# Kernel optimization log

Measured on AMD Instinct MI355X. Metric: run time of the kernel, lower is better.

## Reference

```python
import jax, jax.numpy as jnp
import numpy as np

B, S, IN, H, OUT = 64, 512, 1024, 512, 512
EPS = 1e-5
ADAPTIVE_RATE = 0.01


def setup_inputs() -> dict:
    key = jax.random.key(0)
    ks = iter(jax.random.split(key, 64))

    def rn(shape, scale):
        return (jax.random.normal(next(ks), shape, jnp.float32) * scale)

    d = {}
    d["x"] = jax.random.normal(next(ks), (B, S, IN), jnp.float32)
    d["context"] = jax.random.normal(next(ks), (B, H), jnp.float32)
    d["state_importance"] = jnp.ones((1, H), jnp.float32)
    # embedding
    d["W_emb"], d["b_emb"] = rn((H, IN), 0.02), rn((H,), 0.01)
    # core layers: Linear + BatchNorm1d (gamma=1, beta=0 torch init)
    d["W0"], d["b0"] = rn((H, H), 0.03), rn((H,), 0.01)
    d["g0"], d["bt0"] = jnp.ones((H,), jnp.float32), jnp.zeros((H,), jnp.float32)
    d["W1"], d["b1"] = rn((H, H), 0.03), rn((H,), 0.01)
    d["g1"], d["bt1"] = jnp.ones((H,), jnp.float32), jnp.zeros((H,), jnp.float32)
    # two LSTMCells (hidden -> hidden), torch gate order i,f,g,o
    lstm_scale = 1.0 / np.sqrt(H)
    for l in range(2):
        d[f"Wih{l}"] = rn((4 * H, H), lstm_scale)
        d[f"Whh{l}"] = rn((4 * H, H), lstm_scale)
        d[f"bih{l}"] = rn((4 * H,), lstm_scale)
        d[f"bhh{l}"] = rn((4 * H,), lstm_scale)
    # compression gate: Linear(2H, H) + LayerNorm + Sigmoid
    d["Wc"], d["bc"] = rn((H, 2 * H), 0.02), rn((H,), 0.01)
    d["lnc_g"], d["lnc_b"] = jnp.ones((H,), jnp.float32), jnp.zeros((H,), jnp.float32)
    # importance generator: Linear, ReLU, Linear, LayerNorm, Sigmoid
    d["Wi1"], d["bi1"] = rn((H, H), 0.03), rn((H,), 0.01)
    d["Wi2"], d["bi2"] = rn((H, H), 0.03), rn((H,), 0.01)
    d["lni_g"], d["lni_b"] = jnp.ones((H,), jnp.float32), jnp.zeros((H,), jnp.float32)
    # final layer
    d["Wf"], d["bf"] = rn((OUT, H), 0.03), rn((OUT,), 0.01)
    return d


def _bn_channel_dim1(h, gamma, beta):
    # BatchNorm1d (training mode) on (B, S, H) with channel dim = dim 1 (S == num_features)
    m = h.mean(axis=(0, 2), keepdims=True)
    v = h.var(axis=(0, 2), keepdims=True)  # biased, like torch normalization
    return gamma[None, :, None] * (h - m) / jnp.sqrt(v + EPS) + beta[None, :, None]


def _ln(h, g, b):
    m = h.mean(-1, keepdims=True)
    v = h.var(-1, keepdims=True)
    return g * (h - m) / jnp.sqrt(v + EPS) + b


def _lstm_cell(xt, h, c, Wih, Whh, bih, bhh):
    z = xt @ Wih.T + bih + h @ Whh.T + bhh  # (B, 4H)
    i, f, g, o = jnp.split(z, 4, axis=-1)
    c = jax.nn.sigmoid(f) * c + jax.nn.sigmoid(i) * jnp.tanh(g)
    h = jax.nn.sigmoid(o) * jnp.tanh(c)
    return h, c


def reference(x, context, state_importance, W_emb, b_emb,
              W0, b0, g0, bt0, W1, b1, g1, bt1,
              Wih0, Whh0, bih0, bhh0, Wih1, Whh1, bih1, bhh1,
              Wc, bc, lnc_g, lnc_b, Wi1, bi1, Wi2, bi2, lni_g, lni_b,
              Wf, bf):
    h = x @ W_emb.T + b_emb  # (B, S, H)
    h = jax.nn.relu(_bn_channel_dim1(h @ W0.T + b0, g0, bt0))
    h = jax.nn.relu(_bn_channel_dim1(h @ W1.T + b1, g1, bt1))

    # stacked 2-layer LSTMCell over the sequence, keep only the final hidden
    zeros = jnp.zeros((B, H), h.dtype)

    def step(carry, xt):
        h0, c0, h1, c1 = carry
        h0, c0 = _lstm_cell(xt, h0, c0, Wih0, Whh0, bih0, bhh0)
        h1, c1 = _lstm_cell(h0, h1, c1, Wih1, Whh1, bih1, bhh1)
        return (h0, c0, h1, c1), None

    (h0, c0, h1, c1), _ = jax.lax.scan(step, (zeros, zeros, zeros, zeros),
                                       jnp.swapaxes(h, 0, 1))
    processed = h1  # (B, H)

    comp = jax.nn.sigmoid(_ln(jnp.concatenate([processed, context], axis=-1) @ Wc.T + bc,
                              lnc_g, lnc_b))
    compressed = processed * comp

    imp = jax.nn.sigmoid(_ln(jax.nn.relu(compressed @ Wi1.T + bi1) @ Wi2.T + bi2,
                             lni_g, lni_b))
    si_new = state_importance + ADAPTIVE_RATE * (
        jnp.abs(imp).mean(axis=0, keepdims=True) - state_importance)

    out = compressed @ Wf.T + bf
    return out, si_new
```

## Files before the change

### kernel.cpp

```cpp
#include <hip/hip_runtime.h>
#include <hip/hip_bf16.h>
#include <stdint.h>


typedef __attribute__((ext_vector_type(8))) short short8;
typedef __attribute__((ext_vector_type(4))) float floatx4;
typedef __attribute__((ext_vector_type(2))) unsigned uintx2;

__device__ inline float b2f(short u){
  union { float f; uint32_t i; } x; x.i = ((uint32_t)(uint16_t)u) << 16; return x.f;
}
__device__ inline short f2b(float f){
  union { float f; uint32_t i; } x; x.f = f;
  uint32_t r = (x.i + 0x7FFFu + ((x.i >> 16) & 1u)) >> 16;
  return (short)(uint16_t)r;
}
__device__ inline float sigm(float x){ return 1.0f / (1.0f + __expf(-x)); }

__device__ inline float blk_sum(float v, float* red){
  #pragma unroll
  for (int o = 32; o > 0; o >>= 1) v += __shfl_down(v, o, 64);
  int wv = threadIdx.x >> 6;
  __syncthreads();
  if ((threadIdx.x & 63) == 0) red[wv] = v;
  __syncthreads();
  return red[0] + red[1] + red[2] + red[3];
}

__device__ inline void stage16(const short* g, short* l){
  __builtin_amdgcn_global_load_lds(
      (const __attribute__((address_space(1))) void*)(uintptr_t)g,
      (__attribute__((address_space(3))) void*)(uintptr_t)l,
      16, 0, 0);
}

__device__ inline int ldsLoadAcq(int* p){
  return __hip_atomic_load(p, __ATOMIC_ACQUIRE, __HIP_MEMORY_SCOPE_WORKGROUP);
}
__device__ inline void ldsStoreRel(int* p, int v){
  __hip_atomic_store(p, v, __ATOMIC_RELEASE, __HIP_MEMORY_SCOPE_WORKGROUP);
}
__device__ inline int ldsAddRel(int* p){
  return __hip_atomic_fetch_add(p, 1, __ATOMIC_RELEASE, __HIP_MEMORY_SCOPE_WORKGROUP);
}


__global__ void set_flag(const unsigned* __restrict__ si_bits, unsigned* __restrict__ flag){
  if (threadIdx.x == 0 && blockIdx.x == 0)
    *flag = (si_bits[0] == 0x3F800000u) ? 1u : 0u;
}


__global__ __launch_bounds__(256) void convq(
    const unsigned* __restrict__ flag, int mode,
    const void* s0, long e0, short* d0, int n0,
    const void* s1, long e1, short* d1, int n1,
    const void* s2, long e2, short* d2, int n2,
    const void* s3, long e3, short* d3, int n3)
{
  const bool isf32 = (*flag != 0u);
  const int gid = blockIdx.x*256 + threadIdx.x;
  const int stride = gridDim.x*256;
  const void* ss[4] = {s0,s1,s2,s3};
  long ee[4]  = {e0,e1,e2,e3};
  short* dd[4] = {d0,d1,d2,d3};
  int nn[4]   = {n0,n1,n2,n3};
  for (int s = 0; s < 4; s++){
    if (!dd[s]) continue;
    if (mode == 1) {
      if (!isf32) continue;
      for (int i = gid; i < nn[s]; i += stride)
        dd[s][i] = ((const short*)ss[s])[ee[s] + i];
    } else if (isf32) {
      for (int i = gid; i < nn[s]; i += stride)
        dd[s][i] = f2b(((const float*)ss[s])[ee[s] + i]);
    } else {
      for (int i = gid; i < nn[s]; i += stride)
        dd[s][i] = ((const short*)ss[s])[ee[s] + i];
    }
  }
}


__global__ __launch_bounds__(256) void gemm_bt(
    const short* __restrict__ A, const short* __restrict__ A2, int splitRow,
    int lda, const short* __restrict__ W, const short* __restrict__ bias,
    short* __restrict__ C, int ldc, int row0, int K)
{
  __shared__ alignas(16) short As[128*32];
  __shared__ alignas(16) short Bs[128*32];
  const int tid  = threadIdx.x;
  const int lane = tid & 63;
  const int wave = tid >> 6;
  const int wm = wave >> 1, wn = wave & 1;
  const int bm = blockIdx.x, bn = blockIdx.y;
  const int R0 = row0 + bm*128;
  const short* Ab = (R0 < splitRow) ? A2 : A;

  floatx4 acc[4][4];
  #pragma unroll
  for (int i = 0; i < 4; i++)
    #pragma unroll
    for (int j = 0; j < 4; j++){ floatx4 z = {0.f,0.f,0.f,0.f}; acc[i][j] = z; }

  const short* Ag = Ab + (size_t)(R0 + (tid >> 2))*lda + (tid & 3)*8;
  const short* Wg = W  + (size_t)(bn*128 + (tid >> 2))*K + (tid & 3)*8;

  const int kk  = (lane >> 4) * 8;
  const int rA  = wm*64 + (lane & 15);
  const int rB  = wn*64 + (lane & 15);

  for (int k0 = 0; k0 < K; k0 += 32) {
    __syncthreads();
    stage16(Ag + k0,                  As + tid*8);
    stage16(Ag + k0 + (size_t)64*lda, As + 2048 + tid*8);
    stage16(Wg + k0,                  Bs + tid*8);
    stage16(Wg + k0 + (size_t)64*K,   Bs + 2048 + tid*8);
    __syncthreads();

    short8 af[4], bf[4];
    #pragma unroll
    for (int i = 0; i < 4; i++){
      af[i] = *(const short8*)&As[(rA + i*16)*32 + kk];
      bf[i] = *(const short8*)&Bs[(rB + i*16)*32 + kk];
    }
    #pragma unroll
    for (int i = 0; i < 4; i++)
      #pragma unroll
      for (int j = 0; j < 4; j++)
        acc[i][j] = __builtin_amdgcn_mfma_f32_16x16x32_bf16(af[i], bf[j], acc[i][j], 0, 0, 0);
  }

  const int crow0 = R0 + wm*64 + (lane >> 4)*4;
  const int ccol0 = bn*128 + wn*64;
  #pragma unroll
  for (int i = 0; i < 4; i++){
    #pragma unroll
    for (int j = 0; j < 4; j++){
      int col = ccol0 + j*16 + (lane & 15);
      float bv = b2f(bias[col]);
      #pragma unroll
      for (int r = 0; r < 4; r++){
        int row = crow0 + i*16 + r;
        C[(size_t)row*ldc + col] = f2b(acc[i][j][r] + bv);
      }
    }
  }
}


__global__ __launch_bounds__(256) void bn_relu(
    const short* __restrict__ X, const short* __restrict__ gamma,
    const short* __restrict__ beta, short* __restrict__ Y)
{
  const int s = blockIdx.x, tid = threadIdx.x;
  __shared__ float red[4];
  float s1 = 0.f, s2 = 0.f;
  for (int i = tid; i < 4096; i += 256){
    int b = i >> 6, c = i & 63;
    short8 v = *(const short8*)(X + ((size_t)(b*512 + s))*512 + c*8);
    #pragma unroll
    for (int u = 0; u < 8; u++){ float f = b2f(v[u]); s1 += f; s2 += f*f; }
  }
  s1 = blk_sum(s1, red);
  s2 = blk_sum(s2, red);
  float mean = s1 * (1.f/32768.f);
  float var  = fmaxf(s2 * (1.f/32768.f) - mean*mean, 0.f);
  float sc = b2f(gamma[s]) * rsqrtf(var + 1e-5f);
  float sh = b2f(beta[s]) - mean * sc;
  for (int i = tid; i < 4096; i += 256){
    int b = i >> 6, c = i & 63;
    size_t base = ((size_t)(b*512 + s))*512 + c*8;
    short8 v = *(const short8*)(X + base);
    short8 o;
    #pragma unroll
    for (int u = 0; u < 8; u++){
      float f = b2f(v[u]) * sc + sh;
      o[u] = f2b(fmaxf(f, 0.f));
    }
    *(short8*)(Y + base) = o;
  }
}


__global__ __launch_bounds__(256, 1) void lstm_persist(
    const short* __restrict__ Xseq,
    const short* __restrict__ Wih0, const short* __restrict__ Whh0,
    const short* __restrict__ bih0, const short* __restrict__ bhh0,
    const short* __restrict__ Wih1, const short* __restrict__ Whh1,
    const short* __restrict__ bih1, const short* __restrict__ bhh1,
    short* __restrict__ h0r,
    short* __restrict__ h1r,
    unsigned* __restrict__ f0,
    unsigned* __restrict__ f1,
    unsigned* __restrict__ ep0,
    unsigned* __restrict__ ep1)
{
  const int wg   = blockIdx.x;
  const int tid  = threadIdx.x;
  const int lane = tid & 63;
  const int wave = tid >> 6;

  if (wg == 64){
    if (wave >= 2) return;
    const unsigned* sp = (wave == 0 ? f0 : f1) + lane*16;
    unsigned* dp = (wave == 0 ? ep0 : ep1) + lane*16;
    for (unsigned itv = 1; itv <= 512; ++itv){
      for (;;){
        unsigned v;
        asm volatile("global_load_dword %0, %1, off sc1\n\t"
                     "s_waitcnt vmcnt(0)"
                     : "=v"(v) : "v"(sp) : "memory");
        if (__all((int)(v >= itv))) break;
      }
      asm volatile("global_store_dword %0, %1, off sc0 sc1"
                   :: "v"(dp), "v"(itv) : "memory");
    }
    return;
  }

  const int l15  = lane & 15;
  const int quad = lane >> 4;
  const int kq   = quad * 8;

  __shared__ float zp0[2*2*64*33];
  __shared__ float zp1[2*2*64*33];
  __shared__ alignas(16) short xpf[512];
  __shared__ int go0, go1, zc0, zc1, gc0, gc1;
  #define ZPL0(p,t,r,c) zp0[((((p)*2+(t))*64) + (r))*33 + (c)]
  #define ZPL1(p,t,r,c) zp1[((((p)*2+(t))*64) + (r))*33 + (c)]

  if (tid == 0){ go0 = -1; go1 = -1; zc0 = 0; zc1 = 0; gc0 = 0; gc1 = 0; }
  __syncthreads();

  const short* Wt = (wave==0) ? Wih0 : (wave==1) ? Whh0 : (wave==2) ? Wih1 : Whh1;
  short8 wreg[2][16];
  #pragma unroll
  for (int nt = 0; nt < 2; nt++){
    int g2 = nt*2 + (l15 >> 3);
    int ml = l15 & 7;
    const short* wrow = Wt + (size_t)(g2*512 + wg*8 + ml)*512 + kq;
    #pragma unroll
    for (int kk = 0; kk < 16; kk++)
      wreg[nt][kk] = *(const short8*)(wrow + kk*32);
  }

  const int lp  = wave >> 1;
  const int t2  = tid & 127;
  const int bbg = t2 >> 1;
  const int m4  = (t2 & 1) * 4;
  const short* biA = lp ? bih1 : bih0;
  const short* bhA = lp ? bhh1 : bhh0;
  float bsL[4][4];
  #pragma unroll
  for (int g = 0; g < 4; g++)
    #pragma unroll
    for (int j = 0; j < 4; j++){
      int m = wg*8 + m4 + j;
      bsL[g][j] = b2f(biA[g*512+m]) + b2f(bhA[g*512+m]);
    }
  float cst[4] = {0.f, 0.f, 0.f, 0.f};

  for (int it = 0; it <= 512; ++it){
    const bool act = (wave==0) ? (it < 512)
                   : (wave==1) ? (it >= 1 && it < 512)
                   : (wave==2) ? (it >= 1)
                   :             (it >= 2);

    if (wave == 1 && it >= 1){
      const unsigned want = (unsigned)it;
      const unsigned* p = ep0 + wg*16;
      for (;;){
        unsigned v;
        asm volatile("global_load_dword %0, %1, off sc1\n\t"
                     "s_waitcnt vmcnt(0)"
                     : "=v"(v) : "v"(p) : "memory");
        if (v >= want) break;
      }
      __builtin_amdgcn_sched_barrier(0);
      if (lane == 0) ldsStoreRel(&go0, it);
    }
    if (wave == 3){
      if (it >= 2){
        const unsigned want = (unsigned)it;
        const unsigned* p = ep1 + wg*16;
        for (;;){
          unsigned v;
          asm volatile("global_load_dword %0, %1, off sc1\n\t"
                       "s_waitcnt vmcnt(0)"
                       : "=v"(v) : "v"(p) : "memory");
          if (v >= want) break;
        }
        __builtin_amdgcn_sched_barrier(0);
      }
      if (lane == 0) ldsStoreRel(&go1, it);
    }
    if (wave == 2 && it >= 1){
      while (ldsLoadAcq(&go0) < it) { }
      __builtin_amdgcn_sched_barrier(0);
    }

    floatx4 acc[4][2];
    #pragma unroll
    for (int mt = 0; mt < 4; mt++)
      #pragma unroll
      for (int nt = 0; nt < 2; nt++){ floatx4 z = {0.f,0.f,0.f,0.f}; acc[mt][nt] = z; }

    if (act){
      const short* Ab;
      size_t rstride;
      if (wave == 0)      { Ab = Xseq + (size_t)it*512;               rstride = 262144; }
      else if (wave <= 2) { Ab = h0r + (size_t)((it-1)&1)*32768;      rstride = 512; }
      else                { Ab = h1r + (size_t)(it&1)*32768;          rstride = 512; }
      const short* ap[4];
      #pragma unroll
      for (int mt = 0; mt < 4; mt++)
        ap[mt] = Ab + (size_t)(mt*16 + l15)*rstride + kq;

      if (wave == 0){
        #pragma unroll
        for (int kk = 0; kk < 16; kk++){
          short8 af[4];
          #pragma unroll
          for (int mt = 0; mt < 4; mt++) af[mt] = *(const short8*)(ap[mt] + kk*32);
          #pragma unroll
          for (int mt = 0; mt < 4; mt++){
            acc[mt][0] = __builtin_amdgcn_mfma_f32_16x16x32_bf16(af[mt], wreg[0][kk], acc[mt][0], 0, 0, 0);
            acc[mt][1] = __builtin_amdgcn_mfma_f32_16x16x32_bf16(af[mt], wreg[1][kk], acc[mt][1], 0, 0, 0);
          }
        }
      } else {
        short8 hb[2][4][4];
        #pragma unroll
        for (int pb = 0; pb < 2; pb++)
          #pragma unroll
          for (int kk = 0; kk < 4; kk++)
            #pragma unroll
            for (int mt = 0; mt < 4; mt++)
              asm volatile("global_load_dwordx4 %0, %1, off sc1"
                           : "=v"(hb[pb][kk][mt])
                           : "v"(ap[mt] + (pb*4 + kk)*32));
        #pragma unroll
        for (int kb = 0; kb < 4; kb++){
          const int cur = kb & 1;
          if (kb < 3) asm volatile("s_waitcnt vmcnt(16)" ::: "memory");
          else        asm volatile("s_waitcnt vmcnt(0)"  ::: "memory");
          __builtin_amdgcn_sched_barrier(0);
          #pragma unroll
          for (int kk = 0; kk < 4; kk++)
            #pragma unroll
            for (int mt = 0; mt < 4; mt++){
              acc[mt][0] = __builtin_amdgcn_mfma_f32_16x16x32_bf16(hb[cur][kk][mt], wreg[0][kb*4+kk], acc[mt][0], 0, 0, 0);
              acc[mt][1] = __builtin_amdgcn_mfma_f32_16x16x32_bf16(hb[cur][kk][mt], wreg[1][kb*4+kk], acc[mt][1], 0, 0, 0);
            }
          if (kb < 2){
            #pragma unroll
            for (int kk = 0; kk < 4; kk++)
              #pragma unroll
              for (int mt = 0; mt < 4; mt++)
                asm volatile("global_load_dwordx4 %0, %1, off sc1"
                             : "=v"(hb[cur][kk][mt])
                             : "v"(ap[mt] + ((kb+2)*4 + kk)*32));
          }
        }
      }
    }

    const int par = it & 1;
    if (wave < 2){
      if (it < 512){
        if (it >= 2) while (ldsLoadAcq(&gc0) < 2*(it-1)) { }
        #pragma unroll
        for (int mt = 0; mt < 4; mt++)
          #pragma unroll
          for (int nt = 0; nt < 2; nt++)
            #pragma unroll
            for (int r = 0; r < 4; r++)
              ZPL0(par, wave, mt*16 + quad*4 + r, nt*16 + l15) = acc[mt][nt][r];
        if (lane == 0) ldsAddRel(&zc0);
      }
    } else {
      if (it >= 1){
        if (it >= 3) while (ldsLoadAcq(&gc1) < 2*(it-2)) { }
        #pragma unroll
        for (int mt = 0; mt < 4; mt++)
          #pragma unroll
          for (int nt = 0; nt < 2; nt++)
            #pragma unroll
            for (int r = 0; r < 4; r++)
              ZPL1(par, wave-2, mt*16 + quad*4 + r, nt*16 + l15) = acc[mt][nt][r];
        if (lane == 0) ldsAddRel(&zc1);
      }
    }

    if (wave < 2){
      if (it < 512){
        while (ldsLoadAcq(&zc0) < 2*(it+1)) { }
        if (it >= 2) while (ldsLoadAcq(&go1) < it) { }
        float hv[4];
        #pragma unroll
        for (int j = 0; j < 4; j++){
          int ml = m4 + j;
          float zi = ZPL0(par,0,bbg,      ml) + ZPL0(par,1,bbg,      ml) + bsL[0][j];
          float zf = ZPL0(par,0,bbg,  8 + ml) + ZPL0(par,1,bbg,  8 + ml) + bsL[1][j];
          float zg = ZPL0(par,0,bbg, 16 + ml) + ZPL0(par,1,bbg, 16 + ml) + bsL[2][j];
          float zo = ZPL0(par,0,bbg, 24 + ml) + ZPL0(par,1,bbg, 24 + ml) + bsL[3][j];
          cst[j] = sigm(zf)*cst[j] + sigm(zi)*tanhf(zg);
          hv[j] = sigm(zo)*tanhf(cst[j]);
        }
        uintx2 d;
        d.x = (unsigned)(uint16_t)f2b(hv[0]) | ((unsigned)(uint16_t)f2b(hv[1]) << 16);
        d.y = (unsigned)(uint16_t)f2b(hv[2]) | ((unsigned)(uint16_t)f2b(hv[3]) << 16);
        short* dst = h0r + (size_t)par*32768 + bbg*512 + wg*8 + m4;
        asm volatile("global_store_dwordx2 %0, %1, off sc0 sc1" :: "v"(dst), "v"(d) : "memory");
        asm volatile("s_waitcnt vmcnt(0)" ::: "memory");
        __builtin_amdgcn_sched_barrier(0);
        if (lane == 0){
          int old = ldsAddRel(&gc0);
          if (old == 2*it + 1){
            unsigned nv = (unsigned)(it + 1);
            asm volatile("global_store_dword %0, %1, off sc0 sc1"
                         :: "v"(f0 + wg*16), "v"(nv) : "memory");
          }
        }
      }
      if (wave == 0 && it + 2 < 512){
        const short* nx = Xseq + (size_t)(it + 2)*512 + lane*8;
        #pragma unroll 8
        for (int r = 0; r < 64; ++r)
          stage16(nx + (size_t)r*262144, xpf);
      }
    } else {
      if (it >= 1){
        while (ldsLoadAcq(&zc1) < 2*it) { }
        float hv[4];
        #pragma unroll
        for (int j = 0; j < 4; j++){
          int ml = m4 + j;
          float zi = ZPL1(par,0,bbg,      ml) + ZPL1(par,1,bbg,      ml) + bsL[0][j];
          float zf = ZPL1(par,0,bbg,  8 + ml) + ZPL1(par,1,bbg,  8 + ml) + bsL[1][j];
          float zg = ZPL1(par,0,bbg, 16 + ml) + ZPL1(par,1,bbg, 16 + ml) + bsL[2][j];
          float zo = ZPL1(par,0,bbg, 24 + ml) + ZPL1(par,1,bbg, 24 + ml) + bsL[3][j];
          cst[j] = sigm(zf)*cst[j] + sigm(zi)*tanhf(zg);
          hv[j] = sigm(zo)*tanhf(cst[j]);
        }
        uintx2 d;
        d.x = (unsigned)(uint16_t)f2b(hv[0]) | ((unsigned)(uint16_t)f2b(hv[1]) << 16);
        d.y = (unsigned)(uint16_t)f2b(hv[2]) | ((unsigned)(uint16_t)f2b(hv[3]) << 16);
        short* dst = h1r + (size_t)((it-1)&1)*32768 + bbg*512 + wg*8 + m4;
        asm volatile("global_store_dwordx2 %0, %1, off sc0 sc1" :: "v"(dst), "v"(d) : "memory");
        asm volatile("s_waitcnt vmcnt(0)" ::: "memory");
        __builtin_amdgcn_sched_barrier(0);
        if (lane == 0){
          int old = ldsAddRel(&gc1);
          if (old == 2*it - 1){
            unsigned nv = (unsigned)(it + 1);
            asm volatile("global_store_dword %0, %1, off sc0 sc1"
                         :: "v"(f1 + wg*16), "v"(nv) : "memory");
          }
        }
      }
    }
  }
  #undef ZPL0
  #undef ZPL1
}


__global__ __launch_bounds__(256) void head_gate_out(
    const short* __restrict__ h1, const short* __restrict__ ctx,
    const short* __restrict__ Wc, const short* __restrict__ bc,
    const short* __restrict__ lng, const short* __restrict__ lnb,
    const short* __restrict__ Wf, const short* __restrict__ bfb,
    short* __restrict__ compressed, void* __restrict__ outp,
    const unsigned* __restrict__ flag)
{
  const int b = blockIdx.x, tid = threadIdx.x;
  const bool isf32 = (*flag != 0u);
  __shared__ float xc[1024];
  __shared__ float cv[512];
  __shared__ float red[4];
  for (int i = tid; i < 512; i += 256) xc[i]       = b2f(h1 [b*512 + i]);
  for (int i = tid; i < 512; i += 256) xc[512 + i] = b2f(ctx[b*512 + i]);
  __syncthreads();
  float y[2];
  #pragma unroll
  for (int jj = 0; jj < 2; jj++){
    int j = tid + jj*256;
    const short* wr = Wc + (size_t)j*1024;
    float a = 0.f;
    for (int k = 0; k < 1024; k += 8){
      short8 wv = *(const short8*)(wr + k);
      #pragma unroll
      for (int u = 0; u < 8; u++) a += b2f(wv[u]) * xc[k + u];
    }
    y[jj] = a + b2f(bc[j]);
  }
  float s = blk_sum(y[0] + y[1], red);
  float mean = s * (1.f/512.f);
  float q = (y[0]-mean)*(y[0]-mean) + (y[1]-mean)*(y[1]-mean);
  q = blk_sum(q, red);
  float inv = rsqrtf(q * (1.f/512.f) + 1e-5f);
  #pragma unroll
  for (int jj = 0; jj < 2; jj++){
    int j = tid + jj*256;
    float v = (y[jj]-mean)*inv*b2f(lng[j]) + b2f(lnb[j]);
    float cm = xc[j] * sigm(v);
    cv[j] = cm;
    compressed[(size_t)b*512 + j] = f2b(cm);
  }
  __syncthreads();
  #pragma unroll
  for (int jj = 0; jj < 2; jj++){
    int j = tid + jj*256;
    const short* wr = Wf + (size_t)j*512;
    float a = 0.f;
    for (int k = 0; k < 512; k += 8){
      short8 wv = *(const short8*)(wr + k);
      #pragma unroll
      for (int u = 0; u < 8; u++) a += b2f(wv[u]) * cv[k + u];
    }
    float o = a + b2f(bfb[j]);
    if (isf32) ((float*)outp)[(size_t)b*512 + j] = o;
    else       ((short*)outp)[(size_t)b*512 + j] = f2b(o);
  }
}


__global__ __launch_bounds__(256) void head_imp(
    const short* __restrict__ compressed,
    const short* __restrict__ Wi1, const short* __restrict__ bi1,
    const short* __restrict__ Wi2, const short* __restrict__ bi2,
    const short* __restrict__ lng, const short* __restrict__ lnb,
    float* __restrict__ imp)
{
  const int b = blockIdx.x, tid = threadIdx.x;
  __shared__ float xr[512];
  __shared__ float t1[512];
  __shared__ float red[4];
  for (int i = tid; i < 512; i += 256) xr[i] = b2f(compressed[b*512 + i]);
  __syncthreads();
  #pragma unroll
  for (int jj = 0; jj < 2; jj++){
    int j = tid + jj*256;
    const short* wr = Wi1 + (size_t)j*512;
    float a = 0.f;
    for (int k = 0; k < 512; k += 8){
      short8 wv = *(const short8*)(wr + k);
      #pragma unroll
      for (int u = 0; u < 8; u++) a += b2f(wv[u]) * xr[k + u];
    }
    t1[j] = fmaxf(a + b2f(bi1[j]), 0.f);
  }
  __syncthreads();
  float y[2];
  #pragma unroll
  for (int jj = 0; jj < 2; jj++){
    int j = tid + jj*256;
    const short* wr = Wi2 + (size_t)j*512;
    float a = 0.f;
    for (int k = 0; k < 512; k += 8){
      short8 wv = *(const short8*)(wr + k);
      #pragma unroll
      for (int u = 0; u < 8; u++) a += b2f(wv[u]) * t1[k + u];
    }
    y[jj] = a + b2f(bi2[j]);
  }
  float s = blk_sum(y[0] + y[1], red);
  float mean = s * (1.f/512.f);
  float q = (y[0]-mean)*(y[0]-mean) + (y[1]-mean)*(y[1]-mean);
  q = blk_sum(q, red);
  float inv = rsqrtf(q * (1.f/512.f) + 1e-5f);
  #pragma unroll
  for (int jj = 0; jj < 2; jj++){
    int j = tid + jj*256;
    imp[(size_t)b*512 + j] = sigm((y[jj]-mean)*inv*b2f(lng[j]) + b2f(lnb[j]));
  }
}


__global__ __launch_bounds__(256) void head_si(
    const float* __restrict__ imp, const short* __restrict__ si,
    void* __restrict__ outp, const unsigned* __restrict__ flag)
{
  int tid = threadIdx.x;
  const bool isf32 = (*flag != 0u);
  #pragma unroll
  for (int mm = 0; mm < 2; mm++){
    int m = tid + mm*256;
    float s = 0.f;
    for (int b = 0; b < 64; b++) s += fabsf(imp[(size_t)b*512 + m]);
    float mean = s * (1.f/64.f);
    float sv = b2f(si[m]);
    float o = sv + 0.01f*(mean - sv);
    if (isf32) ((float*)outp)[32768 + m] = o;
    else       ((short*)outp)[32768 + m] = f2b(o);
  }
}


extern "C" void kernel_launch(void* const* d_in, const int* in_sizes, int n_in,
                              void* d_out, int out_size, void* d_ws, size_t ws_size,
                              hipStream_t stream)
{
  (void)in_sizes; (void)n_in; (void)out_size; (void)ws_size;
  char* ws = (char*)d_ws;
  unsigned* f0b    = (unsigned*)(ws);
  unsigned* f1b    = (unsigned*)(ws + 4096);
  unsigned* ep0b   = (unsigned*)(ws + 8192);
  unsigned* ep1b   = (unsigned*)(ws + 12288);
  unsigned* flag   = (unsigned*)(ws + 16384);
  short*    xStage = (short*)(ws + 20480);
  short*    ring   = (short*)(ws + 282624);
  short*    comp   = (short*)(ws + 806912);
  float*    impb   = (float*)(ws + 872448);
  short*    SA     = (short*)(ws + 1003520);

  short* h0r = ring;
  short* h1r = ring + 65536;

  short* aWemb = SA + 0;
  short* aW0   = SA + 524288;
  short* aW1   = SA + 786432;
  short* aWih0 = SA + 1048576;
  short* aWhh0 = SA + 2097152;
  short* aWih1 = SA + 3145728;
  short* aWhh1 = SA + 4194304;
  short* aWc   = SA + 5242880;
  short* aWi1  = SA + 5767168;
  short* aWi2  = SA + 6029312;
  short* aWf   = SA + 6291456;
  short* V     = SA + 6553600;
  short* abemb = V + 0;     short* ab0  = V + 512;   short* ag0  = V + 1024;
  short* abt0  = V + 1536;  short* ab1  = V + 2048;  short* ag1  = V + 2560;
  short* abt1  = V + 3072;  short* abih0= V + 3584;  short* abhh0= V + 5632;
  short* abih1 = V + 7680;  short* abhh1= V + 9728;  short* abc  = V + 11776;
  short* alncg = V + 12288; short* alncb= V + 12800; short* abi1 = V + 13312;
  short* abi2  = V + 13824; short* alnig= V + 14336; short* alnib= V + 14848;
  short* abfb  = V + 15360; short* actx = V + 15872; short* asi  = V + 48640;

  short* xb  = (short*)d_in[0];
  short* hL0 = xb + 16777216;

  hipMemsetAsync(ws, 0, 16384, stream);
  set_flag<<<1, 64, 0, stream>>>((const unsigned*)d_in[2], flag);

  dim3 blk(256);
  convq<<<256, blk, 0, stream>>>(flag, 0,
      d_in[0], 0, xStage, 65536, nullptr,0,nullptr,0, nullptr,0,nullptr,0, nullptr,0,nullptr,0);
  for (long n0 = 65536; n0 < 33554432; n0 <<= 1) {
    int blocks = (int)((n0 + 1023) / 1024); if (blocks > 4096) blocks = 4096;
    convq<<<blocks, blk, 0, stream>>>(flag, 0,
        d_in[0], n0, xb + n0, (int)n0, nullptr,0,nullptr,0, nullptr,0,nullptr,0, nullptr,0,nullptr,0);
  }
  convq<<<64, blk, 0, stream>>>(flag, 1,
      xStage, 0, xb, 65536, nullptr,0,nullptr,0, nullptr,0,nullptr,0, nullptr,0,nullptr,0);

  convq<<<1024, blk, 0, stream>>>(flag, 0,
      d_in[3], 0, aWemb, 524288,  d_in[5], 0, aW0, 262144,
      d_in[9], 0, aW1,   262144,  d_in[21],0, aWc, 524288);
  convq<<<2048, blk, 0, stream>>>(flag, 0,
      d_in[13],0, aWih0, 1048576, d_in[14],0, aWhh0, 1048576,
      d_in[17],0, aWih1, 1048576, d_in[18],0, aWhh1, 1048576);
  convq<<<1024, blk, 0, stream>>>(flag, 0,
      d_in[25],0, aWi1, 262144,   d_in[27],0, aWi2, 262144,
      d_in[31],0, aWf,  262144,   d_in[1], 0, actx, 32768);
  convq<<<8, blk, 0, stream>>>(flag, 0,
      d_in[4], 0, abemb, 512,  d_in[6], 0, ab0, 512,
      d_in[7], 0, ag0,   512,  d_in[8], 0, abt0, 512);
  convq<<<8, blk, 0, stream>>>(flag, 0,
      d_in[10],0, ab1, 512,  d_in[11],0, ag1, 512,
      d_in[12],0, abt1,512,  d_in[22],0, abc, 512);
  convq<<<8, blk, 0, stream>>>(flag, 0,
      d_in[15],0, abih0, 2048,  d_in[16],0, abhh0, 2048,
      d_in[19],0, abih1, 2048,  d_in[20],0, abhh1, 2048);
  convq<<<8, blk, 0, stream>>>(flag, 0,
      d_in[23],0, alncg, 512,  d_in[24],0, alncb, 512,
      d_in[26],0, abi1,  512,  d_in[28],0, abi2,  512);
  convq<<<8, blk, 0, stream>>>(flag, 0,
      d_in[29],0, alnig, 512,  d_in[30],0, alnib, 512,
      d_in[32],0, abfb,  512,  d_in[2], 0, asi,   512);

  gemm_bt<<<dim3(1, 4), blk, 0, stream>>>(xb, xb, 0, 1024, aWemb, abemb,
                                          xStage, 512, 0, 1024);
  for (int r0 = 128; r0 < 32768; r0 <<= 1) {
    gemm_bt<<<dim3(r0/128, 4), blk, 0, stream>>>(xb, xb, 0, 1024, aWemb, abemb,
                                                 xb, 512, r0, 1024);
  }
  gemm_bt<<<dim3(256, 4), blk, 0, stream>>>(xb, xStage, 128, 512, aW0, ab0,
                                            hL0, 512, 0, 512);
  bn_relu<<<512, blk, 0, stream>>>(hL0, ag0, abt0, hL0);
  gemm_bt<<<dim3(256, 4), blk, 0, stream>>>(hL0, hL0, 0, 512, aW1, ab1,
                                            xb, 512, 0, 512);
  bn_relu<<<512, blk, 0, stream>>>(xb, ag1, abt1, xb);

  lstm_persist<<<65, blk, 0, stream>>>(xb, aWih0, aWhh0, abih0, abhh0,
                                       aWih1, aWhh1, abih1, abhh1,
                                       h0r, h1r, f0b, f1b, ep0b, ep1b);

  head_gate_out<<<64, blk, 0, stream>>>(h1r + 32768, actx, aWc, abc, alncg, alncb,
                                        aWf, abfb, comp, d_out, flag);
  head_imp<<<64, blk, 0, stream>>>(comp, aWi1, abi1, aWi2, abi2, alnig, alnib, impb);
  head_si<<<1, blk, 0, stream>>>(impb, asi, d_out, flag);
}
```

Before: 6.796 ms.

## Replace aggregator-block barrier with direct per-wave flag polling in LSTM

Removes the extra relay workgroup that gathered per-block completion flags and rebroadcast epoch counters. Each producing wave now writes its own flag into a transposed flag matrix, and consumer waves poll all 64 blocks' flags directly with vector loads and a wave-wide all-reduce. The h0 ring grows from 2 to 4 slots so the layer-0 writer can run further ahead of the layer-1 reader, which relaxes the h1go wait. This takes one hop off the global barrier latency per step. In exchange, every consumer wave issues more polling traffic and the ring needs more memory.

After: 7.991 ms. +17.6%, slower.

```diff
diff --git a/kernel.cpp b/kernel.cpp
--- a/kernel.cpp
+++ b/kernel.cpp
@@ -191,34 +191,13 @@
     const short* __restrict__ bih1, const short* __restrict__ bhh1,
     short* __restrict__ h0r,
     short* __restrict__ h1r,
-    unsigned* __restrict__ f0,
-    unsigned* __restrict__ f1,
-    unsigned* __restrict__ ep0,
-    unsigned* __restrict__ ep1)
+    unsigned* __restrict__ fblk0,
+    unsigned* __restrict__ fblk1)
 {
   const int wg   = blockIdx.x;
   const int tid  = threadIdx.x;
   const int lane = tid & 63;
   const int wave = tid >> 6;
-
-  if (wg == 64){
-    if (wave >= 2) return;
-    const unsigned* sp = (wave == 0 ? f0 : f1) + lane*16;
-    unsigned* dp = (wave == 0 ? ep0 : ep1) + lane*16;
-    for (unsigned itv = 1; itv <= 512; ++itv){
-      for (;;){
-        unsigned v;
-        asm volatile("global_load_dword %0, %1, off sc1\n\t"
-                     "s_waitcnt vmcnt(0)"
-                     : "=v"(v) : "v"(sp) : "memory");
-        if (__all((int)(v >= itv))) break;
-      }
-      asm volatile("global_store_dword %0, %1, off sc0 sc1"
-                   :: "v"(dp), "v"(itv) : "memory");
-    }
-    return;
-  }
-
   const int l15  = lane & 15;
   const int quad = lane >> 4;
   const int kq   = quad * 8;
@@ -226,11 +205,11 @@
   __shared__ float zp0[2*2*64*33];
   __shared__ float zp1[2*2*64*33];
   __shared__ alignas(16) short xpf[512];
-  __shared__ int go0, go1, zc0, zc1, gc0, gc1;
+  __shared__ int h1go, zc0, zc1, gd0, gd1;
   #define ZPL0(p,t,r,c) zp0[((((p)*2+(t))*64) + (r))*33 + (c)]
   #define ZPL1(p,t,r,c) zp1[((((p)*2+(t))*64) + (r))*33 + (c)]
 
-  if (tid == 0){ go0 = -1; go1 = -1; zc0 = 0; zc1 = 0; gc0 = 0; gc1 = 0; }
+  if (tid == 0){ h1go = -1; zc0 = 0; zc1 = 0; gd0 = 0; gd1 = 0; }
   __syncthreads();
 
   const short* Wt = (wave==0) ? Wih0 : (wave==1) ? Whh0 : (wave==2) ? Wih1 : Whh1;
@@ -261,43 +240,39 @@
     }
   float cst[4] = {0.f, 0.f, 0.f, 0.f};
 
+  const unsigned* poll0 = fblk0 + wg*128 + lane*2;
+  const unsigned* poll1 = fblk1 + wg*128 + lane*2;
+
   for (int it = 0; it <= 512; ++it){
     const bool act = (wave==0) ? (it < 512)
                    : (wave==1) ? (it >= 1 && it < 512)
                    : (wave==2) ? (it >= 1)
                    :             (it >= 2);
 
-    if (wave == 1 && it >= 1){
+    if ((wave == 1 && it >= 1 && it < 512) || (wave == 2 && it >= 1)){
       const unsigned want = (unsigned)it;
-      const unsigned* p = ep0 + wg*16;
       for (;;){
-        unsigned v;
-        asm volatile("global_load_dword %0, %1, off sc1\n\t"
+        uintx2 v;
+        asm volatile("global_load_dwordx2 %0, %1, off sc1\n\t"
                      "s_waitcnt vmcnt(0)"
-                     : "=v"(v) : "v"(p) : "memory");
-        if (v >= want) break;
+                     : "=v"(v) : "v"(poll0) : "memory");
+        if (__all((int)(v.x >= want && v.y >= want))) break;
       }
       __builtin_amdgcn_sched_barrier(0);
-      if (lane == 0) ldsStoreRel(&go0, it);
     }
     if (wave == 3){
       if (it >= 2){
         const unsigned want = (unsigned)it;
-        const unsigned* p = ep1 + wg*16;
         for (;;){
-          unsigned v;
-          asm volatile("global_load_dword %0, %1, off sc1\n\t"
+          uintx2 v;
+          asm volatile("global_load_dwordx2 %0, %1, off sc1\n\t"
                        "s_waitcnt vmcnt(0)"
-                       : "=v"(v) : "v"(p) : "memory");
-          if (v >= want) break;
+                       : "=v"(v) : "v"(poll1) : "memory");
+          if (__all((int)(v.x >= want && v.y >= want))) break;
         }
         __builtin_amdgcn_sched_barrier(0);
       }
-      if (lane == 0) ldsStoreRel(&go1, it);
-    }
-    if (wave == 2 && it >= 1){
-      while (ldsLoadAcq(&go0) < it) { }
-      __builtin_amdgcn_sched_barrier(0);
+      if (lane == 0) ldsStoreRel(&h1go, it);
     }
 
     floatx4 acc[4][2];
@@ -310,7 +285,7 @@
       const short* Ab;
       size_t rstride;
       if (wave == 0)      { Ab = Xseq + (size_t)it*512;               rstride = 262144; }
-      else if (wave <= 2) { Ab = h0r + (size_t)((it-1)&1)*32768;      rstride = 512; }
+      else if (wave <= 2) { Ab = h0r + (size_t)((it-1)&3)*32768;      rstride = 512; }
       else                { Ab = h1r + (size_t)(it&1)*32768;          rstride = 512; }
       const short* ap[4];
       #pragma unroll
@@ -369,7 +344,7 @@
     const int par = it & 1;
     if (wave < 2){
       if (it < 512){
-        if (it >= 2) while (ldsLoadAcq(&gc0) < 2*(it-1)) { }
+        if (it >= 2) while (ldsLoadAcq(&gd0) < 2*(it-1)) { }
         #pragma unroll
         for (int mt = 0; mt < 4; mt++)
           #pragma unroll
@@ -381,7 +356,7 @@
       }
     } else {
       if (it >= 1){
-        if (it >= 3) while (ldsLoadAcq(&gc1) < 2*(it-2)) { }
+        if (it >= 3) while (ldsLoadAcq(&gd1) < 2*(it-2)) { }
         #pragma unroll
         for (int mt = 0; mt < 4; mt++)
           #pragma unroll
@@ -396,7 +371,7 @@
     if (wave < 2){
       if (it < 512){
         while (ldsLoadAcq(&zc0) < 2*(it+1)) { }
-        if (it >= 2) while (ldsLoadAcq(&go1) < it) { }
+        if (it >= 4) while (ldsLoadAcq(&h1go) < it-2) { }
         float hv[4];
         #pragma unroll
         for (int j = 0; j < 4; j++){
@@ -411,18 +386,17 @@
         uintx2 d;
         d.x = (unsigned)(uint16_t)f2b(hv[0]) | ((unsigned)(uint16_t)f2b(hv[1]) << 16);
         d.y = (unsigned)(uint16_t)f2b(hv[2]) | ((unsigned)(uint16_t)f2b(hv[3]) << 16);
-        short* dst = h0r + (size_t)par*32768 + bbg*512 + wg*8 + m4;
+        short* dst = h0r + (size_t)(it&3)*32768 + bbg*512 + wg*8 + m4;
         asm volatile("global_store_dwordx2 %0, %1, off sc0 sc1" :: "v"(dst), "v"(d) : "memory");
         asm volatile("s_waitcnt vmcnt(0)" ::: "memory");
         __builtin_amdgcn_sched_barrier(0);
-        if (lane == 0){
-          int old = ldsAddRel(&gc0);
-          if (old == 2*it + 1){
-            unsigned nv = (unsigned)(it + 1);
-            asm volatile("global_store_dword %0, %1, off sc0 sc1"
-                         :: "v"(f0 + wg*16), "v"(nv) : "memory");
-          }
+        {
+          unsigned nv = (unsigned)(it + 1);
+          unsigned* fp = fblk0 + lane*128 + wg*2 + wave;
+          asm volatile("global_store_dword %0, %1, off sc0 sc1"
+                       :: "v"(fp), "v"(nv) : "memory");
         }
+        if (lane == 0) ldsAddRel(&gd0);
       }
       if (wave == 0 && it + 2 < 512){
         const short* nx = Xseq + (size_t)(it + 2)*512 + lane*8;
@@ -451,14 +425,13 @@
         asm volatile("global_store_dwordx2 %0, %1, off sc0 sc1" :: "v"(dst), "v"(d) : "memory");
         asm volatile("s_waitcnt vmcnt(0)" ::: "memory");
         __builtin_amdgcn_sched_barrier(0);
-        if (lane == 0){
-          int old = ldsAddRel(&gc1);
-          if (old == 2*it - 1){
-            unsigned nv = (unsigned)(it + 1);
-            asm volatile("global_store_dword %0, %1, off sc0 sc1"
-                         :: "v"(f1 + wg*16), "v"(nv) : "memory");
-          }
+        {
+          unsigned nv = (unsigned)(it + 1);
+          unsigned* fp = fblk1 + lane*128 + wg*2 + (wave - 2);
+          asm volatile("global_store_dword %0, %1, off sc0 sc1"
+                       :: "v"(fp), "v"(nv) : "memory");
         }
+        if (lane == 0) ldsAddRel(&gd1);
       }
     }
   }
@@ -605,19 +578,15 @@
 {
   (void)in_sizes; (void)n_in; (void)out_size; (void)ws_size;
   char* ws = (char*)d_ws;
-  unsigned* f0b    = (unsigned*)(ws);
-  unsigned* f1b    = (unsigned*)(ws + 4096);
-  unsigned* ep0b   = (unsigned*)(ws + 8192);
-  unsigned* ep1b   = (unsigned*)(ws + 12288);
-  unsigned* flag   = (unsigned*)(ws + 16384);
-  short*    xStage = (short*)(ws + 20480);
-  short*    ring   = (short*)(ws + 282624);
-  short*    comp   = (short*)(ws + 806912);
-  float*    impb   = (float*)(ws + 872448);
-  short*    SA     = (short*)(ws + 1003520);
-
-  short* h0r = ring;
-  short* h1r = ring + 65536;
+  unsigned* fblk0  = (unsigned*)(ws);
+  unsigned* fblk1  = (unsigned*)(ws + 32768);
+  unsigned* flag   = (unsigned*)(ws + 65536);
+  short*    xStage = (short*)(ws + 69632);
+  short*    h0r    = (short*)(ws + 331776);
+  short*    h1r    = (short*)(ws + 593920);
+  short*    comp   = (short*)(ws + 724992);
+  float*    impb   = (float*)(ws + 790528);
+  short*    SA     = (short*)(ws + 921600);
 
   short* aWemb = SA + 0;
   short* aW0   = SA + 524288;
@@ -642,7 +611,7 @@
   short* xb  = (short*)d_in[0];
   short* hL0 = xb + 16777216;
 
-  hipMemsetAsync(ws, 0, 16384, stream);
+  hipMemsetAsync(ws, 0, 65536, stream);
   set_flag<<<1, 64, 0, stream>>>((const unsigned*)d_in[2], flag);
 
   dim3 blk(256);
@@ -694,9 +663,9 @@
                                             xb, 512, 0, 512);
   bn_relu<<<512, blk, 0, stream>>>(xb, ag1, abt1, xb);
 
-  lstm_persist<<<65, blk, 0, stream>>>(xb, aWih0, aWhh0, abih0, abhh0,
+  lstm_persist<<<64, blk, 0, stream>>>(xb, aWih0, aWhh0, abih0, abhh0,
                                        aWih1, aWhh1, abih1, abhh1,
-                                       h0r, h1r, f0b, f1b, ep0b, ep1b);
+                                       h0r, h1r, fblk0, fblk1);
 
   head_gate_out<<<64, blk, 0, stream>>>(h1r + 32768, actx, aWc, abc, alncg, alncb,
                                         aWf, abfb, comp, d_out, flag);
```

## Use 4-deep h0 ring and contiguous hidden-state tile layout in LSTM

Applied to the files above, without the earlier changes.

Changes the hidden-state ring buffers from row-major (batch x hidden) to a tiled layout where each workgroup's 8-column slice for all batch rows is contiguous, so each workgroup's stores and the MFMA operand loads become more contiguous. The h0 ring is deepened from 2 to 4 slots, which lets layer-0 run up to two steps further ahead of layer-1 before waiting on h1go. This aims to cut inter-layer stall time in the persistent recurrent loop and improve memory coalescing. The risk is that the relaxed dependency is only correct if the slot reuse distance matches the wait condition, and the head kernel's read of h1 must match the new layout.

Result: slower. 6.979 ms (+2.7%).

```diff
diff --git a/kernel.cpp b/kernel.cpp
--- a/kernel.cpp
+++ b/kernel.cpp
@@ -226,11 +226,11 @@
   __shared__ float zp0[2*2*64*33];
   __shared__ float zp1[2*2*64*33];
   __shared__ alignas(16) short xpf[512];
-  __shared__ int go0, go1, zc0, zc1, gc0, gc1;
+  __shared__ int go0, h1go, zc0, zc1, gc0, gc1;
   #define ZPL0(p,t,r,c) zp0[((((p)*2+(t))*64) + (r))*33 + (c)]
   #define ZPL1(p,t,r,c) zp1[((((p)*2+(t))*64) + (r))*33 + (c)]
 
-  if (tid == 0){ go0 = -1; go1 = -1; zc0 = 0; zc1 = 0; gc0 = 0; gc1 = 0; }
+  if (tid == 0){ go0 = -1; h1go = -1; zc0 = 0; zc1 = 0; gc0 = 0; gc1 = 0; }
   __syncthreads();
 
   const short* Wt = (wave==0) ? Wih0 : (wave==1) ? Whh0 : (wave==2) ? Wih1 : Whh1;
@@ -293,7 +293,7 @@
         }
         __builtin_amdgcn_sched_barrier(0);
       }
-      if (lane == 0) ldsStoreRel(&go1, it);
+      if (lane == 0) ldsStoreRel(&h1go, it);
     }
     if (wave == 2 && it >= 1){
       while (ldsLoadAcq(&go0) < it) { }
@@ -307,17 +307,11 @@
       for (int nt = 0; nt < 2; nt++){ floatx4 z = {0.f,0.f,0.f,0.f}; acc[mt][nt] = z; }
 
     if (act){
-      const short* Ab;
-      size_t rstride;
-      if (wave == 0)      { Ab = Xseq + (size_t)it*512;               rstride = 262144; }
-      else if (wave <= 2) { Ab = h0r + (size_t)((it-1)&1)*32768;      rstride = 512; }
-      else                { Ab = h1r + (size_t)(it&1)*32768;          rstride = 512; }
-      const short* ap[4];
-      #pragma unroll
-      for (int mt = 0; mt < 4; mt++)
-        ap[mt] = Ab + (size_t)(mt*16 + l15)*rstride + kq;
-
       if (wave == 0){
+        const short* ap[4];
+        #pragma unroll
+        for (int mt = 0; mt < 4; mt++)
+          ap[mt] = Xseq + (size_t)it*512 + (size_t)(mt*16 + l15)*262144 + kq;
         #pragma unroll
         for (int kk = 0; kk < 16; kk++){
           short8 af[4];
@@ -330,6 +324,13 @@
           }
         }
       } else {
+        const short* Ab = (wave <= 2) ? (h0r + (size_t)((it-1)&3)*32768)
+                                      : (h1r + (size_t)(it&1)*32768);
+        const short* ap[4];
+        #pragma unroll
+        for (int mt = 0; mt < 4; mt++)
+          ap[mt] = Ab + (size_t)quad*512 + (size_t)(mt*16 + l15)*8;
+
         short8 hb[2][4][4];
         #pragma unroll
         for (int pb = 0; pb < 2; pb++)
@@ -339,7 +340,7 @@
             for (int mt = 0; mt < 4; mt++)
               asm volatile("global_load_dwordx4 %0, %1, off sc1"
                            : "=v"(hb[pb][kk][mt])
-                           : "v"(ap[mt] + (pb*4 + kk)*32));
+                           : "v"(ap[mt] + (size_t)(pb*4 + kk)*2048));
         #pragma unroll
         for (int kb = 0; kb < 4; kb++){
           const int cur = kb & 1;
@@ -360,7 +361,7 @@
               for (int mt = 0; mt < 4; mt++)
                 asm volatile("global_load_dwordx4 %0, %1, off sc1"
                              : "=v"(hb[cur][kk][mt])
-                             : "v"(ap[mt] + ((kb+2)*4 + kk)*32));
+                             : "v"(ap[mt] + (size_t)((kb+2)*4 + kk)*2048));
           }
         }
       }
@@ -396,7 +397,7 @@
     if (wave < 2){
       if (it < 512){
         while (ldsLoadAcq(&zc0) < 2*(it+1)) { }
-        if (it >= 2) while (ldsLoadAcq(&go1) < it) { }
+        if (it >= 4) while (ldsLoadAcq(&h1go) < it-2) { }
         float hv[4];
         #pragma unroll
         for (int j = 0; j < 4; j++){
@@ -411,7 +412,7 @@
         uintx2 d;
         d.x = (unsigned)(uint16_t)f2b(hv[0]) | ((unsigned)(uint16_t)f2b(hv[1]) << 16);
         d.y = (unsigned)(uint16_t)f2b(hv[2]) | ((unsigned)(uint16_t)f2b(hv[3]) << 16);
-        short* dst = h0r + (size_t)par*32768 + bbg*512 + wg*8 + m4;
+        short* dst = h0r + (size_t)(it&3)*32768 + wg*512 + bbg*8 + m4;
         asm volatile("global_store_dwordx2 %0, %1, off sc0 sc1" :: "v"(dst), "v"(d) : "memory");
         asm volatile("s_waitcnt vmcnt(0)" ::: "memory");
         __builtin_amdgcn_sched_barrier(0);
@@ -447,7 +448,7 @@
         uintx2 d;
         d.x = (unsigned)(uint16_t)f2b(hv[0]) | ((unsigned)(uint16_t)f2b(hv[1]) << 16);
         d.y = (unsigned)(uint16_t)f2b(hv[2]) | ((unsigned)(uint16_t)f2b(hv[3]) << 16);
-        short* dst = h1r + (size_t)((it-1)&1)*32768 + bbg*512 + wg*8 + m4;
+        short* dst = h1r + (size_t)((it-1)&1)*32768 + wg*512 + bbg*8 + m4;
         asm volatile("global_store_dwordx2 %0, %1, off sc0 sc1" :: "v"(dst), "v"(d) : "memory");
         asm volatile("s_waitcnt vmcnt(0)" ::: "memory");
         __builtin_amdgcn_sched_barrier(0);
@@ -480,7 +481,7 @@
   __shared__ float xc[1024];
   __shared__ float cv[512];
   __shared__ float red[4];
-  for (int i = tid; i < 512; i += 256) xc[i]       = b2f(h1 [b*512 + i]);
+  for (int i = tid; i < 512; i += 256) xc[i]       = b2f(h1[(i >> 3)*512 + b*8 + (i & 7)]);
   for (int i = tid; i < 512; i += 256) xc[512 + i] = b2f(ctx[b*512 + i]);
   __syncthreads();
   float y[2];
@@ -611,13 +612,11 @@
   unsigned* ep1b   = (unsigned*)(ws + 12288);
   unsigned* flag   = (unsigned*)(ws + 16384);
   short*    xStage = (short*)(ws + 20480);
-  short*    ring   = (short*)(ws + 282624);
-  short*    comp   = (short*)(ws + 806912);
-  float*    impb   = (float*)(ws + 872448);
-  short*    SA     = (short*)(ws + 1003520);
-
-  short* h0r = ring;
-  short* h1r = ring + 65536;
+  short*    h0r    = (short*)(ws + 282624);
+  short*    h1r    = (short*)(ws + 544768);
+  short*    comp   = (short*)(ws + 675840);
+  float*    impb   = (float*)(ws + 741376);
+  short*    SA     = (short*)(ws + 872448);
 
   short* aWemb = SA + 0;
   short* aW0   = SA + 524288;
```
